# Optimization experiments

Measured on AMD Instinct MI355X. Metric: run time of the kernel, lower is better.

Reference implementation:

```python
import jax, jax.numpy as jnp
import numpy as np

H, D = 8, 16          # heads, per-head dim (hidden_channels=128)
HID = H * D
N = 200000            # movie nodes
E = 500000            # edges per metapath relation
IN = 256              # input feature dim
CLS = 3               # output classes


def setup_inputs() -> dict:
    key = jax.random.key(0)
    ks = jax.random.split(key, 13)
    return {
        "x_movie": jax.random.normal(ks[0], (N, IN), jnp.float32),
        "W_proj": jax.random.normal(ks[1], (IN, HID), jnp.float32) * 0.05,
        "b_proj": jnp.zeros((HID,), jnp.float32),
        "att_src0": jax.random.normal(ks[2], (H, D), jnp.float32) * 0.1,
        "att_dst0": jax.random.normal(ks[3], (H, D), jnp.float32) * 0.1,
        "att_src1": jax.random.normal(ks[4], (H, D), jnp.float32) * 0.1,
        "att_dst1": jax.random.normal(ks[5], (H, D), jnp.float32) * 0.1,
        "q": jax.random.normal(ks[6], (HID,), jnp.float32) * 0.1,
        "k_w": jax.random.normal(ks[7], (HID, HID), jnp.float32) * 0.05,
        "k_b": jnp.zeros((HID,), jnp.float32),
        "lin_w": jax.random.normal(ks[8], (HID, CLS), jnp.float32) * 0.05,
        "lin_b": jnp.zeros((CLS,), jnp.float32),
        "e0_src": jax.random.randint(ks[9], (E,), 0, N, jnp.int32),
        "e0_dst": jax.random.randint(ks[10], (E,), 0, N, jnp.int32),
        "e1_src": jax.random.randint(ks[11], (E,), 0, N, jnp.int32),
        "e1_dst": jax.random.randint(ks[12], (E,), 0, N, jnp.int32),
    }


def _han_rel(h, att_s, att_d, src, dst, n):
    # h: [N, H, D]; GAT-style per-relation attention with segment softmax over dst
    a_s = jnp.sum(h * att_s, axis=-1)                      # [N, H]
    a_d = jnp.sum(h * att_d, axis=-1)                      # [N, H]
    alpha = jax.nn.leaky_relu(a_s[src] + a_d[dst], 0.2)    # [E, H]
    m = jax.ops.segment_max(alpha, dst, num_segments=n)    # per-dst max
    ex = jnp.exp(alpha - m[dst])
    den = jax.ops.segment_sum(ex, dst, num_segments=n)
    w = ex / (den[dst] + 1e-16)                            # edge softmax (PyG eps)
    msg = (h[src] * w[:, :, None]).reshape(-1, HID)        # [E, HID]
    return jax.nn.relu(jax.ops.segment_sum(msg, dst, num_segments=n))


def reference(x_movie, W_proj, b_proj, att_src0, att_dst0, att_src1, att_dst1,
              q, k_w, k_b, lin_w, lin_b, e0_src, e0_dst, e1_src, e1_dst):
    # node-type projection (HANConv.proj), dropout omitted (eval mode)
    h = (x_movie @ W_proj + b_proj).reshape(-1, H, D)      # [N, H, D]
    out0 = _han_rel(h, att_src0, att_dst0, e0_src, e0_dst, N)  # [N, HID]
    out1 = _han_rel(h, att_src1, att_dst1, e1_src, e1_dst, N)
    # semantic-level attention (HANConv.group)
    outs = jnp.stack([out0, out1])                         # [M=2, N, HID]
    score = jnp.sum(jnp.tanh(outs @ k_w + k_b).mean(axis=1) * q, axis=-1)  # [M]
    beta = jax.nn.softmax(score)
    fused = jnp.einsum('m,mnf->nf', beta, outs)            # [N, HID]
    return fused @ lin_w + lin_b                           # [N, CLS]
```

## Files before the change

kernel.cpp:

```cpp
#include <hip/hip_runtime.h>


typedef __attribute__((ext_vector_type(8))) short bf16x8;
typedef __attribute__((ext_vector_type(4))) float f32x4;
typedef __attribute__((ext_vector_type(8))) unsigned short ushort8;

__device__ __forceinline__ unsigned short f2b(float f) {
  union { float f; unsigned u; } v; v.f = f;
  unsigned r = v.u + 0x7fffu + ((v.u >> 16) & 1u);
  return (unsigned short)(r >> 16);
}
__device__ __forceinline__ float b2f(unsigned short u) {
  union { unsigned u; float f; } v; v.u = ((unsigned)u) << 16;
  return v.f;
}
__device__ __forceinline__ float fast_tanh(float x) {
  x = fminf(fmaxf(x, -15.f), 15.f);
  float t = __expf(2.f * x);
  return 1.f - 2.f / (t + 1.f);
}
__device__ __forceinline__ void gload_lds16(const void* g, void* l) {
  __builtin_amdgcn_global_load_lds(
      (const __attribute__((address_space(1))) unsigned int*)g,
      (__attribute__((address_space(3))) unsigned int*)l, 16, 0, 0);
}

__global__ __launch_bounds__(256) void prep_lite(
    const int* __restrict__ e0d, const int* __restrict__ e1d,
    int* __restrict__ deg, int ne, int n,
    const float* __restrict__ Wp, const float* __restrict__ kwm,
    unsigned short* __restrict__ Wpf, unsigned short* __restrict__ Kwf) {
  const int tid = threadIdx.x;
  int b = blockIdx.x;
  const int cb = (2 * ne + 255) >> 8;
  if (b < cb) {
    int e = b * 256 + tid;
    if (e < ne) atomicAdd(&deg[e0d[e]], 1);
    else if (e < 2 * ne) atomicAdd(&deg[n + e1d[e - ne]], 1);
    return;
  }
  b -= cb;
  int t = b * 256 + tid;
  const float* W; unsigned short* Wf; int idx;
  if (t < 4096) { W = Wp; Wf = Wpf; idx = t; }
  else if (t < 6144) { W = kwm; Wf = Kwf; idx = t - 4096; }
  else return;
  int lane = idx & 63, nt = (idx >> 6) & 7, kt = idx >> 9;
  int c = lane & 15, ks = lane >> 4;
  int kbase = kt * 32 + ks * 8;
  int col = nt * 16 + c;
  ushort8 o;
#pragma unroll
  for (int j = 0; j < 8; ++j) o[j] = f2b(W[(size_t)(kbase + j) * 128 + col]);
  *(ushort8*)(Wf + (size_t)idx * 8) = o;
}

__global__ __launch_bounds__(256) void proj_mfma(
    const float* __restrict__ X, const unsigned short* __restrict__ Wf,
    const float* __restrict__ bias,
    const float* __restrict__ as0v, const float* __restrict__ ad0v,
    const float* __restrict__ as1v, const float* __restrict__ ad1v,
    unsigned short* __restrict__ Hb, float* __restrict__ preb, int n) {
  __shared__ float buf[2][4096];
  const int tid = threadIdx.x;
  const int wid = tid >> 6, lane = tid & 63;
  const int wm = wid >> 1, wn = wid & 1;
  const int row0 = blockIdx.x * 64;
  const int r = lane & 15, ks = lane >> 4;

  f32x4 acc[2][4] = {};
  const unsigned short* bptr = Wf + ((size_t)(wn * 4) * 64 + lane) * 8;

#define STAGE(b, s)                                                            \
  {                                                                            \
    _Pragma("unroll")                                                          \
    for (int i = 0; i < 4; ++i) {                                              \
      int rloc = wid * 16 + i * 4 + ks;                                        \
      int grow = row0 + rloc;                                                  \
      grow = grow < n ? grow : n - 1;                                          \
      const float* src =                                                       \
          X + (size_t)grow * 256 + (s) * 64 + ((r ^ (rloc & 7)) << 2);         \
      gload_lds16(src, &buf[b][(wid * 16 + i * 4) * 64]);                      \
    }                                                                          \
  }

#define COMPUTE(b, s)                                                          \
  {                                                                            \
    _Pragma("unroll")                                                          \
    for (int kt = 0; kt < 2; ++kt) {                                           \
      bf16x8 a[2], bb[4];                                                      \
      _Pragma("unroll")                                                        \
      for (int mi = 0; mi < 2; ++mi) {                                         \
        int rr = wm * 32 + mi * 16 + r;                                        \
        const float* lrow = &buf[b][rr * 64];                                  \
        int c0 = kt * 8 + ks * 2;                                              \
        int sw = rr & 7;                                                       \
        float4 f0 = *(const float4*)(lrow + ((c0 ^ sw) * 4));                  \
        float4 f1 = *(const float4*)(lrow + (((c0 + 1) ^ sw) * 4));            \
        bf16x8 v;                                                              \
        v[0] = (short)f2b(f0.x); v[1] = (short)f2b(f0.y);                      \
        v[2] = (short)f2b(f0.z); v[3] = (short)f2b(f0.w);                      \
        v[4] = (short)f2b(f1.x); v[5] = (short)f2b(f1.y);                      \
        v[6] = (short)f2b(f1.z); v[7] = (short)f2b(f1.w);                      \
        a[mi] = v;                                                             \
      }                                                                        \
      _Pragma("unroll")                                                        \
      for (int ni = 0; ni < 4; ++ni)                                           \
        bb[ni] = *(const bf16x8*)(bptr + (((size_t)(s) * 2 + kt) * 8 + ni) * 512); \
      _Pragma("unroll")                                                        \
      for (int mi = 0; mi < 2; ++mi)                                           \
        _Pragma("unroll")                                                      \
        for (int ni = 0; ni < 4; ++ni)                                         \
          acc[mi][ni] = __builtin_amdgcn_mfma_f32_16x16x32_bf16(               \
              a[mi], bb[ni], acc[mi][ni], 0, 0, 0);                            \
    }                                                                          \
  }

  STAGE(0, 0);
  __syncthreads();
  STAGE(1, 1); COMPUTE(0, 0); __syncthreads();
  STAGE(0, 2); COMPUTE(1, 1); __syncthreads();
  STAGE(1, 3); COMPUTE(0, 2); __syncthreads();
  COMPUTE(1, 3);
  __syncthreads();
#undef STAGE
#undef COMPUTE

  unsigned short* ct = (unsigned short*)&buf[0][0];
#pragma unroll
  for (int ni = 0; ni < 4; ++ni) {
    const int col = wn * 64 + ni * 16 + r;
    const float bv = bias[col];
#pragma unroll
    for (int mi = 0; mi < 2; ++mi)
#pragma unroll
      for (int i = 0; i < 4; ++i)
        ct[(wm * 32 + mi * 16 + ks * 4 + i) * 136 + col] = f2b(acc[mi][ni][i] + bv);
  }
  __syncthreads();

  {
    int row = tid >> 2, qq = tid & 3;
    int grow = row0 + row;
    if (grow < n) {
      ushort8* dst = (ushort8*)(Hb + (size_t)grow * 128 + qq * 32);
#pragma unroll
      for (int j = 0; j < 4; ++j) dst[j] = *(ushort8*)&ct[row * 136 + qq * 32 + j * 8];
    }
  }

  const size_t n8 = (size_t)n * 8;
  for (int rh = tid; rh < 512; rh += 256) {
    int row = rh >> 3, head = rh & 7;
    int node = row0 + row;
    if (node < n) {
      float hv[16];
#pragma unroll
      for (int j = 0; j < 16; ++j) hv[j] = b2f(ct[row * 136 + head * 16 + j]);
      float s0 = 0, d0 = 0, s1 = 0, d1 = 0;
      const float* p0 = as0v + head * 16;
      const float* p1 = ad0v + head * 16;
      const float* p2 = as1v + head * 16;
      const float* p3 = ad1v + head * 16;
#pragma unroll
      for (int j = 0; j < 16; ++j) {
        float v = hv[j];
        s0 += v * p0[j]; d0 += v * p1[j];
        s1 += v * p2[j]; d1 += v * p3[j];
      }
      size_t idx = (size_t)node * 8 + head;
      preb[idx] = s0;
      preb[n8 + idx] = d0;
      preb[2 * n8 + idx] = s1;
      preb[3 * n8 + idx] = d1;
    }
  }
}

__global__ __launch_bounds__(256) void scan1_kernel(
    const int* __restrict__ deg, int* __restrict__ pre, int* __restrict__ bsum, int m) {
  __shared__ int sd[256];
  int t = threadIdx.x;
  int base = blockIdx.x * 2048 + t * 8;
  int v[8], sum = 0;
#pragma unroll
  for (int j = 0; j < 8; ++j) {
    v[j] = (base + j < m) ? deg[base + j] : 0;
    sum += v[j];
  }
  sd[t] = sum;
  __syncthreads();
  for (int off = 1; off < 256; off <<= 1) {
    int x = (t >= off) ? sd[t - off] : 0;
    __syncthreads();
    if (t >= off) sd[t] += x;
    __syncthreads();
  }
  if (t == 255) bsum[blockIdx.x] = sd[255];
  int run = sd[t] - sum;
#pragma unroll
  for (int j = 0; j < 8; ++j) {
    if (base + j < m) pre[base + j] = run;
    run += v[j];
  }
}

__global__ __launch_bounds__(256) void scan2_kernel(int* __restrict__ bsum, int nb) {
  __shared__ int sd[256];
  int t = threadIdx.x;
  int v = (t < nb) ? bsum[t] : 0;
  sd[t] = v;
  __syncthreads();
  for (int off = 1; off < 256; off <<= 1) {
    int x = (t >= off) ? sd[t - off] : 0;
    __syncthreads();
    if (t >= off) sd[t] += x;
    __syncthreads();
  }
  if (t < nb) bsum[t] = sd[t] - v;
}

__global__ void scan3_kernel(int* __restrict__ pre, const int* __restrict__ bsum, int m, int total) {
  int i = blockIdx.x * 256 + threadIdx.x;
  if (i < m) pre[i] += bsum[i >> 11];
  if (i == m) pre[m] = total;
}

__global__ void fill2_kernel(const int* __restrict__ e0s, const int* __restrict__ e0d,
                             const int* __restrict__ e1s, const int* __restrict__ e1d,
                             const int* __restrict__ pre, int* __restrict__ cur,
                             int* __restrict__ csr, int ne, int n) {
  int e = blockIdx.x * 256 + threadIdx.x;
  int s, idx;
  if (e < ne) { idx = e0d[e]; s = e0s[e]; }
  else if (e < 2 * ne) { idx = n + e1d[e - ne]; s = e1s[e - ne]; }
  else return;
  int slot = pre[idx] + atomicAdd(&cur[idx], 1);
  csr[slot] = s;
}

__global__ __launch_bounds__(256) void aggscore_mfma(
    const int* __restrict__ pre, const int* __restrict__ csr,
    const unsigned short* __restrict__ Hb, const float* __restrict__ preb,
    const unsigned short* __restrict__ Kf, const float* __restrict__ kb,
    const float* __restrict__ q, const float* __restrict__ lw,
    float* __restrict__ pout, float* __restrict__ sb, int n) {
  __shared__ unsigned short at[16384];
  __shared__ float red[256];
  const int rel = blockIdx.y;
  const int tid = threadIdx.x;
  const int row0 = blockIdx.x * 128;
  const size_t n8 = (size_t)n * 8;
  const float* a_s = preb + (size_t)(2 * rel) * n8;
  const float* a_d = preb + (size_t)(2 * rel + 1) * n8;

  {
    const int lane8 = tid & 7;
    const int nsub = tid >> 3;
#pragma unroll
    for (int it = 0; it < 4; ++it) {
      int row = it * 32 + nsub;
      int node = row0 + row;
      float s = 0.f;
      float acc[16] = {};
      if (node < n) {
        int beg = pre[rel * n + node], end = pre[rel * n + node + 1];
        float ad = a_d[(size_t)node * 8 + lane8];
        int e = beg;
        for (; e + 1 < end; e += 2) {
          int s0 = csr[e], s1 = csr[e + 1];
          float al0 = a_s[(size_t)s0 * 8 + lane8] + ad;
          float al1 = a_s[(size_t)s1 * 8 + lane8] + ad;
          const ushort8* h0p = (const ushort8*)(Hb + (size_t)s0 * 128 + lane8 * 16);
          const ushort8* h1p = (const ushort8*)(Hb + (size_t)s1 * 128 + lane8 * 16);
          ushort8 h0a = h0p[0], h0b = h0p[1];
          ushort8 h1a = h1p[0], h1b = h1p[1];
          al0 = (al0 >= 0.f) ? al0 : 0.2f * al0;
          al1 = (al1 >= 0.f) ? al1 : 0.2f * al1;
          float p0 = __expf(al0), p1 = __expf(al1);
          s += p0 + p1;
#pragma unroll
          for (int j = 0; j < 8; ++j) {
            acc[j]     += p0 * b2f(h0a[j]) + p1 * b2f(h1a[j]);
            acc[8 + j] += p0 * b2f(h0b[j]) + p1 * b2f(h1b[j]);
          }
        }
        if (e < end) {
          int s0 = csr[e];
          float al0 = a_s[(size_t)s0 * 8 + lane8] + ad;
          const ushort8* h0p = (const ushort8*)(Hb + (size_t)s0 * 128 + lane8 * 16);
          ushort8 h0a = h0p[0], h0b = h0p[1];
          al0 = (al0 >= 0.f) ? al0 : 0.2f * al0;
          float p0 = __expf(al0);
          s += p0;
#pragma unroll
          for (int j = 0; j < 8; ++j) {
            acc[j]     += p0 * b2f(h0a[j]);
            acc[8 + j] += p0 * b2f(h0b[j]);
          }
        }
      }
      float inv = 1.f / (s + 1e-16f);
      ushort8 o0, o1;
#pragma unroll
      for (int j = 0; j < 8; ++j) {
        o0[j] = f2b(fmaxf(acc[j] * inv, 0.f));
        o1[j] = f2b(fmaxf(acc[8 + j] * inv, 0.f));
      }
      int sw = row & 7;
      *(ushort8*)&at[row * 128 + (((lane8 * 2) ^ sw) * 8)] = o0;
      *(ushort8*)&at[row * 128 + (((lane8 * 2 + 1) ^ sw) * 8)] = o1;
    }
  }
  __syncthreads();

  const int wid = tid >> 6, lane = tid & 63;
  const int wm = wid >> 1, wn = wid & 1;
  const int r = lane & 15, ks = lane >> 4;
  f32x4 acc[4][4] = {};
  const unsigned short* bptr = Kf + ((size_t)(wn * 4) * 64 + lane) * 8;
#pragma unroll
  for (int kt = 0; kt < 4; ++kt) {
    bf16x8 a[4], b[4];
#pragma unroll
    for (int mi = 0; mi < 4; ++mi) {
      int row = wm * 64 + mi * 16 + r;
      a[mi] = *(const bf16x8*)&at[row * 128 + (((kt * 4 + ks) ^ (row & 7)) * 8)];
    }
#pragma unroll
    for (int ni = 0; ni < 4; ++ni)
      b[ni] = *(const bf16x8*)(bptr + ((size_t)kt * 8 + ni) * 512);
#pragma unroll
    for (int mi = 0; mi < 4; ++mi)
#pragma unroll
      for (int ni = 0; ni < 4; ++ni)
        acc[mi][ni] = __builtin_amdgcn_mfma_f32_16x16x32_bf16(a[mi], b[ni], acc[mi][ni], 0, 0, 0);
  }

  if (tid < 128) {
    int node = row0 + tid;
    if (node < n) {
      float p0 = 0.f, p1 = 0.f, p2 = 0.f;
      int s = tid & 7;
#pragma unroll
      for (int c = 0; c < 16; ++c) {
        const unsigned short* rp = &at[tid * 128 + ((c ^ s) * 8)];
#pragma unroll
        for (int j = 0; j < 8; ++j) {
          float v = b2f(rp[j]);
          const float* w = lw + (size_t)(c * 8 + j) * 3;
          p0 += v * w[0]; p1 += v * w[1]; p2 += v * w[2];
        }
      }
      float4 o = make_float4(p0, p1, p2, 0.f);
      *(float4*)(pout + (size_t)node * 8 + rel * 4) = o;
    }
  }

  float part = 0.f;
#pragma unroll
  for (int ni = 0; ni < 4; ++ni) {
    const int col = wn * 64 + ni * 16 + r;
    const float kbv = kb[col], qv = q[col];
#pragma unroll
    for (int mi = 0; mi < 4; ++mi) {
#pragma unroll
      for (int i = 0; i < 4; ++i) {
        int row = row0 + wm * 64 + mi * 16 + ks * 4 + i;
        if (row < n) part += fast_tanh(acc[mi][ni][i] + kbv) * qv;
      }
    }
  }
  red[tid] = part;
  __syncthreads();
  for (int off = 128; off > 0; off >>= 1) {
    if (tid < off) red[tid] += red[tid + off];
    __syncthreads();
  }
  if (tid == 0) atomicAdd(&sb[rel], red[0]);
}

__global__ void beta_kernel(float* __restrict__ sb, float invn) {
  if (threadIdx.x == 0 && blockIdx.x == 0) {
    float s0 = sb[0] * invn, s1 = sb[1] * invn;
    float m = fmaxf(s0, s1);
    float e0 = __expf(s0 - m), e1 = __expf(s1 - m);
    float d = e0 + e1;
    sb[2] = e0 / d;
    sb[3] = e1 / d;
  }
}

__global__ __launch_bounds__(256) void final2_kernel(
    const float* __restrict__ pout, const float* __restrict__ sb,
    const float* __restrict__ lb, float* __restrict__ out, int n) {
  int node = blockIdx.x * 256 + threadIdx.x;
  if (node >= n) return;
  float b0 = sb[2], b1 = sb[3];
  const float4* p = (const float4*)(pout + (size_t)node * 8);
  float4 pa = p[0], pb = p[1];
  float* d = out + (size_t)node * 3;
  d[0] = b0 * pa.x + b1 * pb.x + lb[0];
  d[1] = b0 * pa.y + b1 * pb.y + lb[1];
  d[2] = b0 * pa.z + b1 * pb.z + lb[2];
}

extern "C" void kernel_launch(void* const* d_in, const int* in_sizes, int n_in,
                              void* d_out, int out_size, void* d_ws, size_t ws_size,
                              hipStream_t stream) {
  const float* x   = (const float*)d_in[0];
  const float* Wp  = (const float*)d_in[1];
  const float* bp  = (const float*)d_in[2];
  const float* as0 = (const float*)d_in[3];
  const float* ad0 = (const float*)d_in[4];
  const float* as1 = (const float*)d_in[5];
  const float* ad1 = (const float*)d_in[6];
  const float* q   = (const float*)d_in[7];
  const float* kw  = (const float*)d_in[8];
  const float* kb  = (const float*)d_in[9];
  const float* lw  = (const float*)d_in[10];
  const float* lb  = (const float*)d_in[11];
  const int* e0s = (const int*)d_in[12];
  const int* e0d = (const int*)d_in[13];
  const int* e1s = (const int*)d_in[14];
  const int* e1d = (const int*)d_in[15];
  const int n  = in_sizes[0] / 256;
  const int ne = in_sizes[12];
  float* out = (float*)d_out;

  char* ws = (char*)d_ws;
  size_t off = 0;
  auto alloc = [&](size_t b) -> char* {
    char* p = ws + off;
    off = (off + b + 255) & ~(size_t)255;
    return p;
  };
  unsigned short* h    = (unsigned short*)alloc((size_t)n * 128 * 2);
  float* preb = (float*)alloc((size_t)4 * n * 8 * 4);
  float* pout = (float*)alloc((size_t)n * 8 * 4);
  int* pre    = (int*)alloc((size_t)(2 * n + 1) * 4);
  int* csr    = (int*)alloc((size_t)2 * ne * 4);
  int* deg    = (int*)alloc(((size_t)4 * n + 4) * 4);
  int* cur    = deg + 2 * n;
  float* sb   = (float*)(deg + 4 * n);
  int* bsum   = (int*)alloc(256 * 4);
  unsigned short* Wpf = (unsigned short*)alloc((size_t)4096 * 8 * 2);
  unsigned short* Kwf = (unsigned short*)alloc((size_t)2048 * 8 * 2);

  const int m = 2 * n;
  const int nblk_scan = (m + 2047) / 2048;
  const int cnt_blks = (2 * ne + 255) / 256;

  hipMemsetAsync(deg, 0, ((size_t)4 * n + 4) * 4, stream);
  hipLaunchKernelGGL(prep_lite, dim3(cnt_blks + 24), dim3(256), 0, stream,
                     e0d, e1d, deg, ne, n, Wp, kw, Wpf, Kwf);

  const int gproj = (n + 63) / 64;
  hipLaunchKernelGGL(proj_mfma, dim3(gproj), dim3(256), 0, stream,
                     x, Wpf, bp, as0, ad0, as1, ad1, h, preb, n);

  hipLaunchKernelGGL(scan1_kernel, dim3(nblk_scan), dim3(256), 0, stream, deg, pre, bsum, m);
  hipLaunchKernelGGL(scan2_kernel, dim3(1), dim3(256), 0, stream, bsum, nblk_scan);
  hipLaunchKernelGGL(scan3_kernel, dim3((m + 1 + 255) / 256), dim3(256), 0, stream,
                     pre, bsum, m, 2 * ne);
  hipLaunchKernelGGL(fill2_kernel, dim3((2 * ne + 255) / 256), dim3(256), 0, stream,
                     e0s, e0d, e1s, e1d, pre, cur, csr, ne, n);

  hipLaunchKernelGGL(aggscore_mfma, dim3((n + 127) / 128, 2), dim3(256), 0, stream,
                     pre, csr, h, preb, Kwf, kb, q, lw, pout, sb, n);
  hipLaunchKernelGGL(beta_kernel, dim3(1), dim3(64), 0, stream, sb, 1.0f / n);
  hipLaunchKernelGGL(final2_kernel, dim3((n + 255) / 256), dim3(256), 0, stream,
                     pout, sb, lb, out, n);
}
```

Measured before the change: 320.8 us.

## Prefetch projection weights into registers and widen aggregation blocks to 512 threads

The projection GEMM now loads each stage's B fragments into double-buffered register arrays one stage ahead. It replaces __syncthreads with explicit vmcnt waits and scheduling barriers, so global weight loads overlap the MFMA work of the previous stage. The aggregation/score kernel moves to 512-thread blocks. The gather phase is split across twice as many threads, and the class-logit dot products run on separate waves concurrently with the MFMA score waves. This adds register pressure and relies on hand-counted vmcnt values for correctness.

```diff
diff --git a/kernel.cpp b/kernel.cpp
--- a/kernel.cpp
+++ b/kernel.cpp
@@ -70,6 +70,15 @@
 
   f32x4 acc[2][4] = {};
   const unsigned short* bptr = Wf + ((size_t)(wn * 4) * 64 + lane) * 8;
+  bf16x8 Br0[8], Br1[8];
+
+#define VMWAIT(N) asm volatile("s_waitcnt vmcnt(" #N ")" ::: "memory")
+#define SBAR()                                                                 \
+  {                                                                            \
+    __builtin_amdgcn_sched_barrier(0);                                         \
+    __builtin_amdgcn_s_barrier();                                              \
+    __builtin_amdgcn_sched_barrier(0);                                         \
+  }
 
 #define STAGE(b, s)                                                            \
   {                                                                            \
@@ -84,11 +93,19 @@
     }                                                                          \
   }
 
-#define COMPUTE(b, s)                                                          \
+#define BLOAD(P, s)                                                            \
+  {                                                                            \
+    _Pragma("unroll")                                                          \
+    for (int j = 0; j < 8; ++j)                                                \
+      P[j] = *(const bf16x8*)(bptr +                                           \
+                (((size_t)(s) * 2 + (j >> 2)) * 8 + (j & 3)) * 512);           \
+  }
+
+#define COMPUTE_R(b, P)                                                        \
   {                                                                            \
     _Pragma("unroll")                                                          \
     for (int kt = 0; kt < 2; ++kt) {                                           \
-      bf16x8 a[2], bb[4];                                                      \
+      bf16x8 a[2];                                                             \
       _Pragma("unroll")                                                        \
       for (int mi = 0; mi < 2; ++mi) {                                         \
         int rr = wm * 32 + mi * 16 + r;                                        \
@@ -105,26 +122,40 @@
         a[mi] = v;                                                             \
       }                                                                        \
       _Pragma("unroll")                                                        \
-      for (int ni = 0; ni < 4; ++ni)                                           \
-        bb[ni] = *(const bf16x8*)(bptr + (((size_t)(s) * 2 + kt) * 8 + ni) * 512); \
-      _Pragma("unroll")                                                        \
-      for (int mi = 0; mi < 2; ++mi)                                           \
-        _Pragma("unroll")                                                      \
-        for (int ni = 0; ni < 4; ++ni)                                         \
-          acc[mi][ni] = __builtin_amdgcn_mfma_f32_16x16x32_bf16(               \
-              a[mi], bb[ni], acc[mi][ni], 0, 0, 0);                            \
+      for (int ni = 0; ni < 4; ++ni) {                                         \
+        acc[0][ni] = __builtin_amdgcn_mfma_f32_16x16x32_bf16(                  \
+            a[0], P[kt * 4 + ni], acc[0][ni], 0, 0, 0);                        \
+        acc[1][ni] = __builtin_amdgcn_mfma_f32_16x16x32_bf16(                  \
+            a[1], P[kt * 4 + ni], acc[1][ni], 0, 0, 0);                        \
+      }                                                                        \
     }                                                                          \
   }
 
   STAGE(0, 0);
-  __syncthreads();
-  STAGE(1, 1); COMPUTE(0, 0); __syncthreads();
-  STAGE(0, 2); COMPUTE(1, 1); __syncthreads();
-  STAGE(1, 3); COMPUTE(0, 2); __syncthreads();
-  COMPUTE(1, 3);
+  BLOAD(Br0, 0);
+  STAGE(1, 1);
+  VMWAIT(4); SBAR();
+  BLOAD(Br1, 1);
+  COMPUTE_R(0, Br0);
+  SBAR();
+  STAGE(0, 2);
+  VMWAIT(4); SBAR();
+  BLOAD(Br0, 2);
+  COMPUTE_R(1, Br1);
+  SBAR();
+  STAGE(1, 3);
+  VMWAIT(4); SBAR();
+  BLOAD(Br1, 3);
+  COMPUTE_R(0, Br0);
+  SBAR();
+  VMWAIT(0); SBAR();
+  COMPUTE_R(1, Br1);
   __syncthreads();
 #undef STAGE
-#undef COMPUTE
+#undef BLOAD
+#undef COMPUTE_R
+#undef VMWAIT
+#undef SBAR
 
   unsigned short* ct = (unsigned short*)&buf[0][0];
 #pragma unroll
@@ -239,14 +270,14 @@
   csr[slot] = s;
 }
 
-__global__ __launch_bounds__(256) void aggscore_mfma(
+__global__ __launch_bounds__(512) void aggscore_mfma(
     const int* __restrict__ pre, const int* __restrict__ csr,
     const unsigned short* __restrict__ Hb, const float* __restrict__ preb,
     const unsigned short* __restrict__ Kf, const float* __restrict__ kb,
     const float* __restrict__ q, const float* __restrict__ lw,
     float* __restrict__ pout, float* __restrict__ sb, int n) {
   __shared__ unsigned short at[16384];
-  __shared__ float red[256];
+  __shared__ float red[512];
   const int rel = blockIdx.y;
   const int tid = threadIdx.x;
   const int row0 = blockIdx.x * 128;
@@ -258,8 +289,8 @@
     const int lane8 = tid & 7;
     const int nsub = tid >> 3;
 #pragma unroll
-    for (int it = 0; it < 4; ++it) {
-      int row = it * 32 + nsub;
+    for (int it = 0; it < 2; ++it) {
+      int row = it * 64 + nsub;
       int node = row0 + row;
       float s = 0.f;
       float acc[16] = {};
@@ -314,37 +345,53 @@
   }
   __syncthreads();
 
-  const int wid = tid >> 6, lane = tid & 63;
-  const int wm = wid >> 1, wn = wid & 1;
-  const int r = lane & 15, ks = lane >> 4;
-  f32x4 acc[4][4] = {};
-  const unsigned short* bptr = Kf + ((size_t)(wn * 4) * 64 + lane) * 8;
-#pragma unroll
-  for (int kt = 0; kt < 4; ++kt) {
-    bf16x8 a[4], b[4];
-#pragma unroll
-    for (int mi = 0; mi < 4; ++mi) {
-      int row = wm * 64 + mi * 16 + r;
-      a[mi] = *(const bf16x8*)&at[row * 128 + (((kt * 4 + ks) ^ (row & 7)) * 8)];
+  const int wid = tid >> 6;
+  float part = 0.f;
+  if (wid < 4) {
+    const int lane = tid & 63;
+    const int wm = wid >> 1, wn = wid & 1;
+    const int r = lane & 15, ks = lane >> 4;
+    f32x4 acc[4][4] = {};
+    const unsigned short* bptr = Kf + ((size_t)(wn * 4) * 64 + lane) * 8;
+#pragma unroll
+    for (int kt = 0; kt < 4; ++kt) {
+      bf16x8 a[4], b[4];
+#pragma unroll
+      for (int mi = 0; mi < 4; ++mi) {
+        int row = wm * 64 + mi * 16 + r;
+        a[mi] = *(const bf16x8*)&at[row * 128 + (((kt * 4 + ks) ^ (row & 7)) * 8)];
+      }
+#pragma unroll
+      for (int ni = 0; ni < 4; ++ni)
+        b[ni] = *(const bf16x8*)(bptr + ((size_t)kt * 8 + ni) * 512);
+#pragma unroll
+      for (int mi = 0; mi < 4; ++mi)
+#pragma unroll
+        for (int ni = 0; ni < 4; ++ni)
+          acc[mi][ni] = __builtin_amdgcn_mfma_f32_16x16x32_bf16(a[mi], b[ni], acc[mi][ni], 0, 0, 0);
     }
 #pragma unroll
-    for (int ni = 0; ni < 4; ++ni)
-      b[ni] = *(const bf16x8*)(bptr + ((size_t)kt * 8 + ni) * 512);
-#pragma unroll
-    for (int mi = 0; mi < 4; ++mi)
-#pragma unroll
-      for (int ni = 0; ni < 4; ++ni)
-        acc[mi][ni] = __builtin_amdgcn_mfma_f32_16x16x32_bf16(a[mi], b[ni], acc[mi][ni], 0, 0, 0);
-  }
-
-  if (tid < 128) {
-    int node = row0 + tid;
+    for (int ni = 0; ni < 4; ++ni) {
+      const int col = wn * 64 + ni * 16 + r;
+      const float kbv = kb[col], qv = q[col];
+#pragma unroll
+      for (int mi = 0; mi < 4; ++mi) {
+#pragma unroll
+        for (int i = 0; i < 4; ++i) {
+          int row = row0 + wm * 64 + mi * 16 + ks * 4 + i;
+          if (row < n) part += fast_tanh(acc[mi][ni][i] + kbv) * qv;
+        }
+      }
+    }
+  } else if (tid < 384) {
+    int t2 = tid - 256;
+    int node = row0 + t2;
     if (node < n) {
       float p0 = 0.f, p1 = 0.f, p2 = 0.f;
-      int s = tid & 7;
+      int s = t2 & 7;
 #pragma unroll
       for (int c = 0; c < 16; ++c) {
-        const unsigned short* rp = &at[tid * 128 + ((c ^ s) * 8)];
+        const unsigned short* rp = &at[t2 * 128 + ((c ^ s) * 8)];
 #pragma unroll
         for (int j = 0; j < 8; ++j) {
           float v = b2f(rp[j]);
@@ -356,24 +403,9 @@
       *(float4*)(pout + (size_t)node * 8 + rel * 4) = o;
     }
   }
-
-  float part = 0.f;
-#pragma unroll
-  for (int ni = 0; ni < 4; ++ni) {
-    const int col = wn * 64 + ni * 16 + r;
-    const float kbv = kb[col], qv = q[col];
-#pragma unroll
-    for (int mi = 0; mi < 4; ++mi) {
-#pragma unroll
-      for (int i = 0; i < 4; ++i) {
-        int row = row0 + wm * 64 + mi * 16 + ks * 4 + i;
-        if (row < n) part += fast_tanh(acc[mi][ni][i] + kbv) * qv;
-      }
-    }
-  }
   red[tid] = part;
   __syncthreads();
-  for (int off = 128; off > 0; off >>= 1) {
+  for (int off = 256; off > 0; off >>= 1) {
     if (tid < off) red[tid] += red[tid + off];
     __syncthreads();
   }
@@ -466,7 +498,7 @@
   hipLaunchKernelGGL(fill2_kernel, dim3((2 * ne + 255) / 256), dim3(256), 0, stream,
                      e0s, e0d, e1s, e1d, pre, cur, csr, ne, n);
 
-  hipLaunchKernelGGL(aggscore_mfma, dim3((n + 127) / 128, 2), dim3(256), 0, stream,
+  hipLaunchKernelGGL(aggscore_mfma, dim3((n + 127) / 128, 2), dim3(512), 0, stream,
                      pre, csr, h, preb, Kwf, kb, q, lw, pout, sb, n);
   hipLaunchKernelGGL(beta_kernel, dim3(1), dim3(64), 0, stream, sb, 1.0f / n);
   hipLaunchKernelGGL(final2_kernel, dim3((n + 255) / 256), dim3(256), 0, stream,
```

New measurement: 301.4 us. 1.06x faster.
